# Kernel optimization log

Hardware: AMD Instinct MI355X
Metric: run time of the kernel (lower is better)

The kernel has to match this reference:

```python
import jax, jax.numpy as jnp
import numpy as np

B, T, N = 8, 1024, 1024
R, NR = 8, 128          # regions, neurons per region (N = R*NR)
D = 512                 # d_model


def setup_inputs() -> dict:
    key = jax.random.key(0)
    ks = jax.random.split(key, 6)
    spikes = jax.random.normal(ks[0], (B, T, N), dtype=jnp.float32)
    # region assignment: random permutation of neuron ids split into R groups
    perm = jax.random.permutation(ks[1], N)
    region_indices = perm.reshape(R, NR).astype(jnp.int32)
    # per-region Linear(NR -> D) stored already transposed for gathered layout
    W_enc = jax.random.normal(ks[2], (R, NR, D), dtype=jnp.float32) / np.sqrt(NR)
    b_enc = jax.random.normal(ks[3], (R, D), dtype=jnp.float32) * 0.02
    # per-region Linear(D -> NR)
    W_dec = jax.random.normal(ks[4], (R, D, NR), dtype=jnp.float32) / np.sqrt(D)
    b_dec = jax.random.normal(ks[5], (R, NR), dtype=jnp.float32) * 0.02
    return {"spikes": spikes, "W_enc": W_enc, "b_enc": b_enc,
            "W_dec": W_dec, "b_dec": b_dec, "region_indices": region_indices}


def reference(spikes, W_enc, b_enc, W_dec, b_dec, region_indices):
    # gather: per-region channel subsets  [B,T,R,NR]
    x_r = spikes[:, :, region_indices]
    # RegionEncoder: Linear(NR -> D) per region  [B,T,R,D]
    tokens = jnp.einsum('btrn,rnd->btrd', x_r, W_enc) + b_enc
    # RegionDecoder: Linear(D -> NR) per region  [B,T,R,NR]
    y = jnp.einsum('btrd,rdn->btrn', tokens, W_dec) + b_dec
    # scatter back into full neuron axis (index_copy_ on dim 2)
    flat_idx = region_indices.reshape(-1)          # [N], a permutation
    out = jnp.zeros_like(spikes).at[:, :, flat_idx].set(y.reshape(spikes.shape[0], spikes.shape[1], -1))
    return out
```

## Files before the change

### kernel.cpp

```cpp
#include <hip/hip_runtime.h>
#include <hip/hip_bf16.h>


typedef __attribute__((ext_vector_type(8))) short bf16x8;
typedef __attribute__((ext_vector_type(4))) float f32x4;
typedef __attribute__((ext_vector_type(4))) short s16x4;

#define NREG 8
#define NRD  128
#define DD   512
#define NN   1024
#define ROWS 16

static __device__ __forceinline__ unsigned short f2bf(float x) {
  union { float f; unsigned u; } v; v.f = x;
  unsigned r = v.u + 0x7fffu + ((v.u >> 16) & 1u);
  return (unsigned short)(r >> 16);
}
static __device__ __forceinline__ unsigned short f2bf_hw(float x) {
  union { __hip_bfloat16 h; unsigned short u; } c;
  c.h = __float2bfloat16(x);
  return c.u;
}
static __device__ __forceinline__ float bf2f(unsigned short b) {
  union { unsigned u; float f; } v; v.u = ((unsigned)b) << 16;
  return v.f;
}

__global__ __launch_bounds__(256) void prep1_kernel(
    const float* __restrict__ W_enc, const float* __restrict__ b_enc,
    const float* __restrict__ W_dec, const int* __restrict__ idx,
    int* __restrict__ pos_ws, float* __restrict__ part,
    float* __restrict__ part_c)
{
  __shared__ unsigned short As[128 * 128];
  __shared__ unsigned short Bs[128 * 128];
  int blk = blockIdx.x, t = threadIdx.x;

  if (blk < 32) {
    int r = blk >> 2, dc = blk & 3, d0 = dc * 128;
    const float* We = W_enc + (size_t)r * NRD * DD;
    const float* Wd = W_dec + (size_t)r * DD * NRD;
    const float* be = b_enc + (size_t)r * DD;

    int n4 = (t & 31) * 4, dlb = t >> 5;
    float c0 = 0.f, c1 = 0.f, c2 = 0.f, c3 = 0.f;
    #pragma unroll
    for (int p = 0; p < 16; ++p) {
      int dl = dlb + p * 8;
      float4 v = *(const float4*)&Wd[(size_t)(d0 + dl) * NRD + n4];
      float bev = be[d0 + dl];
      As[(n4 + 0) * 128 + (dl ^ (((n4 + 0) & 7) << 3))] = f2bf(v.x);
      As[(n4 + 1) * 128 + (dl ^ (((n4 + 1) & 7) << 3))] = f2bf(v.y);
      As[(n4 + 2) * 128 + (dl ^ (((n4 + 2) & 7) << 3))] = f2bf(v.z);
      As[(n4 + 3) * 128 + (dl ^ (((n4 + 3) & 7) << 3))] = f2bf(v.w);
      c0 += v.x * bev; c1 += v.y * bev; c2 += v.z * bev; c3 += v.w * bev;
    }
    {
      float4 cv; cv.x = c0; cv.y = c1; cv.z = c2; cv.w = c3;
      *(float4*)&part_c[((size_t)(r * 4 + dc) * 8 + dlb) * 128 + n4] = cv;
    }
    #pragma unroll
    for (int i = 0; i < 8; ++i) {
      int cid = t + i * 256;
      int k = cid >> 4, dq = (cid & 15) * 8;
      const float* src = &We[(size_t)k * DD + d0 + dq];
      float4 u = *(const float4*)src;
      float4 u2 = *(const float4*)(src + 4);
      bf16x8 pk;
      pk[0] = (short)f2bf(u.x);  pk[1] = (short)f2bf(u.y);
      pk[2] = (short)f2bf(u.z);  pk[3] = (short)f2bf(u.w);
      pk[4] = (short)f2bf(u2.x); pk[5] = (short)f2bf(u2.y);
      pk[6] = (short)f2bf(u2.z); pk[7] = (short)f2bf(u2.w);
      *(bf16x8*)&Bs[k * 128 + (dq ^ ((k & 7) << 3))] = pk;
    }
    __syncthreads();

    int lane = t & 63, w = t >> 6;
    int arow = lane & 15, ag = lane >> 4;
    f32x4 acc[8][2];
    #pragma unroll
    for (int i = 0; i < 8; ++i) {
      acc[i][0] = (f32x4){0.f, 0.f, 0.f, 0.f};
      acc[i][1] = (f32x4){0.f, 0.f, 0.f, 0.f};
    }
    #pragma unroll
    for (int nt = 0; nt < 8; ++nt) {
      int nl = nt * 16 + arow, asw = (nl & 7) << 3;
      bf16x8 a[4];
      #pragma unroll
      for (int ks = 0; ks < 4; ++ks)
        a[ks] = *(const bf16x8*)&As[nl * 128 + ((ks * 32 + ag * 8) ^ asw)];
      #pragma unroll
      for (int kt = 0; kt < 2; ++kt) {
        int kk = w * 32 + kt * 16 + arow, bsw = (kk & 7) << 3;
        #pragma unroll
        for (int ks = 0; ks < 4; ++ks) {
          bf16x8 b = *(const bf16x8*)&Bs[kk * 128 + ((ks * 32 + ag * 8) ^ bsw)];
          acc[nt][kt] = __builtin_amdgcn_mfma_f32_16x16x32_bf16(a[ks], b, acc[nt][kt], 0, 0, 0);
        }
      }
    }
    float* dst = part + (size_t)(r * 4 + dc) * 16384;
    #pragma unroll
    for (int nt = 0; nt < 8; ++nt)
      #pragma unroll
      for (int kt = 0; kt < 2; ++kt)
        #pragma unroll
        for (int v = 0; v < 4; ++v)
          dst[(nt * 16 + ag * 4 + v) * 128 + (w * 32 + kt * 16 + arow)] = acc[nt][kt][v];
  } else {
    #pragma unroll
    for (int i = 0; i < 4; ++i) {
      int q = t * 4 + i;
      pos_ws[idx[q]] = q;
    }
  }
}

__global__ __launch_bounds__(256) void prep2_kernel(
    const float* __restrict__ part, const float* __restrict__ part_c,
    const float* __restrict__ b_dec, unsigned short* __restrict__ MTp,
    float* __restrict__ c_ws)
{
  int blk = blockIdx.x, t = threadIdx.x;
  if (blk < 128) {
    int e0 = (blk * 256 + t) * 4;
    int r = e0 >> 14, off = e0 & 16383;
    int n = off >> 7, k0 = off & 127;
    const float* p = part + (size_t)r * 4 * 16384 + off;
    float4 s0 = *(const float4*)&p[0];
    float4 s1 = *(const float4*)&p[16384];
    float4 s2 = *(const float4*)&p[32768];
    float4 s3 = *(const float4*)&p[49152];
    s16x4 o;
    o.x = (short)f2bf(s0.x + s1.x + s2.x + s3.x);
    o.y = (short)f2bf(s0.y + s1.y + s2.y + s3.y);
    o.z = (short)f2bf(s0.z + s1.z + s2.z + s3.z);
    o.w = (short)f2bf(s0.w + s1.w + s2.w + s3.w);
    int w = n >> 4, arow = n & 15, kt = k0 >> 5, ag = (k0 >> 3) & 3, sub = k0 & 7;
    int chunk = (r * 32 + w * 4 + kt) * 64 + (arow * 4 + ag);
    *(s16x4*)&MTp[chunk * 8 + sub] = o;
  } else if (blk < 132) {
    int e = (blk - 128) * 256 + t;
    int n = e & 127;
    int r = e >> 7;
    float s = b_dec[e];
    #pragma unroll
    for (int dc = 0; dc < 4; ++dc)
      #pragma unroll
      for (int g = 0; g < 8; ++g)
        s += part_c[((size_t)(r * 4 + dc) * 8 + g) * 128 + n];
    c_ws[e] = s;
  }
}

__global__ __launch_bounds__(512, 4) void codec_kernel(
    const float* __restrict__ spikes, const int* __restrict__ pos_ws,
    const float* __restrict__ c_ws, const unsigned short* __restrict__ MTp,
    float* __restrict__ out)
{
  __shared__ unsigned short Xs[ROWS * NN];
  int t = threadIdx.x;
  int w = t >> 6, lane = t & 63;
  int arow = lane & 15, ag = lane >> 4;
  int asw = (arow & 7) << 3;
  int lanechunk = arow * 4 + ag;
  size_t row0 = (size_t)blockIdx.x * ROWS;
  const bf16x8* Bb = (const bf16x8*)MTp;

  int4 p4c[4];
  #pragma unroll
  for (int ch = 0; ch < 4; ++ch)
    p4c[ch] = *(const int4*)&pos_ws[ch * 256 + lane * 4];
  float cvr[8];
  #pragma unroll
  for (int j = 0; j < 8; ++j)
    cvr[j] = c_ws[w * 128 + j * 16 + arow];

  float4 sv[4][2];
  #pragma unroll
  for (int ch = 0; ch < 4; ++ch)
    #pragma unroll
    for (int rl = 0; rl < 2; ++rl)
      sv[ch][rl] = *(const float4*)&spikes[(row0 + w * 2 + rl) * NN + ch * 256 + lane * 4];

  bf16x8 bb[2][4];
  #pragma unroll
  for (int kt = 0; kt < 4; ++kt)
    bb[0][kt] = Bb[(w * 32 + 0 * 4 + kt) * 64 + lanechunk];
  #pragma unroll
  for (int kt = 0; kt < 4; ++kt)
    bb[1][kt] = Bb[(w * 32 + 1 * 4 + kt) * 64 + lanechunk];

  #pragma unroll
  for (int ch = 0; ch < 4; ++ch) {
    int4 p4 = p4c[ch];
    #pragma unroll
    for (int rl = 0; rl < 2; ++rl) {
      int row = w * 2 + rl;
      int base = row * NN, sw = (row & 7) << 3;
      float4 v = sv[ch][rl];
      Xs[base + (p4.x ^ sw)] = f2bf_hw(v.x);
      Xs[base + (p4.y ^ sw)] = f2bf_hw(v.y);
      Xs[base + (p4.z ^ sw)] = f2bf_hw(v.z);
      Xs[base + (p4.w ^ sw)] = f2bf_hw(v.w);
    }
  }
  __syncthreads();

  bf16x8 a[4];
  #pragma unroll
  for (int kt = 0; kt < 4; ++kt)
    a[kt] = *(const bf16x8*)&Xs[arow * NN + ((w * 128 + kt * 32 + ag * 8) ^ asw)];
  #pragma unroll
  for (int j = 0; j < 8; ++j) {
    f32x4 acc = {0.f, 0.f, 0.f, 0.f};
    #pragma unroll
    for (int kt = 0; kt < 4; ++kt)
      acc = __builtin_amdgcn_mfma_f32_16x16x32_bf16(a[kt], bb[j & 1][kt], acc, 0, 0, 0);
    if (j + 2 < 8) {
      #pragma unroll
      for (int kt = 0; kt < 4; ++kt)
        bb[j & 1][kt] = Bb[(w * 32 + (j + 2) * 4 + kt) * 64 + lanechunk];
    }
    int coln = w * 128 + j * 16 + arow;
    #pragma unroll
    for (int v = 0; v < 4; ++v) {
      int i = ag * 4 + v, isw = (i & 7) << 3;
      Xs[i * NN + (coln ^ isw)] = f2bf_hw(acc[v] + cvr[j]);
    }
  }
  __syncthreads();

  #pragma unroll
  for (int ch = 0; ch < 4; ++ch) {
    int j = ch * 256 + lane * 4;
    int4 p4 = p4c[ch];
    #pragma unroll
    for (int rl = 0; rl < 2; ++rl) {
      int row = w * 2 + rl;
      int base = row * NN, sw = (row & 7) << 3;
      float4 v;
      v.x = bf2f(Xs[base + (p4.x ^ sw)]);
      v.y = bf2f(Xs[base + (p4.y ^ sw)]);
      v.z = bf2f(Xs[base + (p4.z ^ sw)]);
      v.w = bf2f(Xs[base + (p4.w ^ sw)]);
      *(float4*)&out[(row0 + row) * NN + j] = v;
    }
  }
}

extern "C" void kernel_launch(void* const* d_in, const int* in_sizes, int n_in,
                              void* d_out, int out_size, void* d_ws, size_t ws_size,
                              hipStream_t stream) {
  const float* spikes = (const float*)d_in[0];
  const float* W_enc  = (const float*)d_in[1];
  const float* b_enc  = (const float*)d_in[2];
  const float* W_dec  = (const float*)d_in[3];
  const float* b_dec  = (const float*)d_in[4];
  const int*   idx    = (const int*)d_in[5];
  float* out = (float*)d_out;

  char* ws = (char*)d_ws;
  int*            pos_ws  = (int*)ws;
  float*          c_ws    = (float*)(ws + 4096);
  unsigned short* MTp_ws  = (unsigned short*)(ws + 8192);
  float*          part    = (float*)(ws + 270336);
  float*          part_c  = (float*)(ws + 2367488);

  prep1_kernel<<<33, 256, 0, stream>>>(W_enc, b_enc, W_dec, idx,
                                       pos_ws, part, part_c);
  prep2_kernel<<<132, 256, 0, stream>>>(part, part_c, b_dec, MTp_ws, c_ws);
  codec_kernel<<<8192 / ROWS, 512, 0, stream>>>(spikes, pos_ws, c_ws, MTp_ws, out);
}
```

Before: 31.91 us.

## Stage raw fp32 spikes in LDS via direct loads and gather at MFMA operand read

The codec kernel now copies each spike row straight into LDS as fp32 with global_load_lds. It then does the neuron-permutation gather while building the bf16 MFMA A operands, using region_indices directly instead of an inverse-permutation scatter. Decoder outputs are kept as fp32 in LDS at their scattered positions and streamed out with vector copies, which removes the per-element bf16 scatter and the bf16 round-trip on output. The cost is a doubled LDS footprint per block (64KB), which may cut the number of resident blocks per CU.

Result: slower. 32.78 us (+2.7%).

```diff
diff --git a/kernel.cpp b/kernel.cpp
--- a/kernel.cpp
+++ b/kernel.cpp
@@ -21,10 +21,6 @@
   union { __hip_bfloat16 h; unsigned short u; } c;
   c.h = __float2bfloat16(x);
   return c.u;
-}
-static __device__ __forceinline__ float bf2f(unsigned short b) {
-  union { unsigned u; float f; } v; v.u = ((unsigned)b) << 16;
-  return v.f;
 }
 
 __global__ __launch_bounds__(256) void prep1_kernel(
@@ -127,7 +123,6 @@
   if (blk < 128) {
     int e0 = (blk * 256 + t) * 4;
     int r = e0 >> 14, off = e0 & 16383;
-    int n = off >> 7, k0 = off & 127;
     const float* p = part + (size_t)r * 4 * 16384 + off;
     float4 s0 = *(const float4*)&p[0];
     float4 s1 = *(const float4*)&p[16384];
@@ -138,6 +133,7 @@
     o.y = (short)f2bf(s0.y + s1.y + s2.y + s3.y);
     o.z = (short)f2bf(s0.z + s1.z + s2.z + s3.z);
     o.w = (short)f2bf(s0.w + s1.w + s2.w + s3.w);
+    int n = off >> 7, k0 = off & 127;
     int w = n >> 4, arow = n & 15, kt = k0 >> 5, ag = (k0 >> 3) & 3, sub = k0 & 7;
     int chunk = (r * 32 + w * 4 + kt) * 64 + (arow * 4 + ag);
     *(s16x4*)&MTp[chunk * 8 + sub] = o;
@@ -156,35 +152,49 @@
 }
 
 __global__ __launch_bounds__(512, 4) void codec_kernel(
-    const float* __restrict__ spikes, const int* __restrict__ pos_ws,
+    const float* __restrict__ spikes, const int* __restrict__ idx,
     const float* __restrict__ c_ws, const unsigned short* __restrict__ MTp,
     float* __restrict__ out)
 {
-  __shared__ unsigned short Xs[ROWS * NN];
+  __shared__ float Xs[ROWS * NN];
   int t = threadIdx.x;
   int w = t >> 6, lane = t & 63;
   int arow = lane & 15, ag = lane >> 4;
-  int asw = (arow & 7) << 3;
+  int aswz = (arow & 7) << 2;
   int lanechunk = arow * 4 + ag;
   size_t row0 = (size_t)blockIdx.x * ROWS;
   const bf16x8* Bb = (const bf16x8*)MTp;
-
-  int4 p4c[4];
-  #pragma unroll
-  for (int ch = 0; ch < 4; ++ch)
-    p4c[ch] = *(const int4*)&pos_ws[ch * 256 + lane * 4];
+  const int* idxr = idx + w * 128;
+
+  #pragma unroll
+  for (int rl = 0; rl < 2; ++rl) {
+    int row = w * 2 + rl;
+    int sw = (row & 7) << 2;
+    const float* srow = &spikes[(row0 + row) * NN];
+    float* drow = &Xs[row * NN];
+    #pragma unroll
+    for (int ch = 0; ch < 4; ++ch) {
+      int u = ch * 256 + lane * 4;
+      __builtin_amdgcn_global_load_lds(
+          (const __attribute__((address_space(1))) void*)&srow[u ^ sw],
+          (__attribute__((address_space(3))) void*)&drow[ch * 256],
+          16, 0, 0);
+    }
+  }
+
+  int4 iv[4][2];
+  #pragma unroll
+  for (int kt = 0; kt < 4; ++kt) {
+    iv[kt][0] = *(const int4*)&idxr[kt * 32 + ag * 8];
+    iv[kt][1] = *(const int4*)&idxr[kt * 32 + ag * 8 + 4];
+  }
+  int colv[8];
   float cvr[8];
   #pragma unroll
-  for (int j = 0; j < 8; ++j)
-    cvr[j] = c_ws[w * 128 + j * 16 + arow];
-
-  float4 sv[4][2];
-  #pragma unroll
-  for (int ch = 0; ch < 4; ++ch)
-    #pragma unroll
-    for (int rl = 0; rl < 2; ++rl)
-      sv[ch][rl] = *(const float4*)&spikes[(row0 + w * 2 + rl) * NN + ch * 256 + lane * 4];
-
+  for (int j = 0; j < 8; ++j) {
+    colv[j] = idxr[j * 16 + arow];
+    cvr[j]  = c_ws[w * 128 + j * 16 + arow];
+  }
   bf16x8 bb[2][4];
   #pragma unroll
   for (int kt = 0; kt < 4; ++kt)
@@ -193,26 +203,25 @@
   for (int kt = 0; kt < 4; ++kt)
     bb[1][kt] = Bb[(w * 32 + 1 * 4 + kt) * 64 + lanechunk];
 
-  #pragma unroll
-  for (int ch = 0; ch < 4; ++ch) {
-    int4 p4 = p4c[ch];
-    #pragma unroll
-    for (int rl = 0; rl < 2; ++rl) {
-      int row = w * 2 + rl;
-      int base = row * NN, sw = (row & 7) << 3;
-      float4 v = sv[ch][rl];
-      Xs[base + (p4.x ^ sw)] = f2bf_hw(v.x);
-      Xs[base + (p4.y ^ sw)] = f2bf_hw(v.y);
-      Xs[base + (p4.z ^ sw)] = f2bf_hw(v.z);
-      Xs[base + (p4.w ^ sw)] = f2bf_hw(v.w);
-    }
-  }
   __syncthreads();
 
+  const float* arow_p = &Xs[arow * NN];
   bf16x8 a[4];
   #pragma unroll
-  for (int kt = 0; kt < 4; ++kt)
-    a[kt] = *(const bf16x8*)&Xs[arow * NN + ((w * 128 + kt * 32 + ag * 8) ^ asw)];
+  for (int kt = 0; kt < 4; ++kt) {
+    int4 i0 = iv[kt][0], i1 = iv[kt][1];
+    bf16x8 pk;
+    pk[0] = (short)f2bf_hw(arow_p[i0.x ^ aswz]);
+    pk[1] = (short)f2bf_hw(arow_p[i0.y ^ aswz]);
+    pk[2] = (short)f2bf_hw(arow_p[i0.z ^ aswz]);
+    pk[3] = (short)f2bf_hw(arow_p[i0.w ^ aswz]);
+    pk[4] = (short)f2bf_hw(arow_p[i1.x ^ aswz]);
+    pk[5] = (short)f2bf_hw(arow_p[i1.y ^ aswz]);
+    pk[6] = (short)f2bf_hw(arow_p[i1.z ^ aswz]);
+    pk[7] = (short)f2bf_hw(arow_p[i1.w ^ aswz]);
+    a[kt] = pk;
+  }
+
   #pragma unroll
   for (int j = 0; j < 8; ++j) {
     f32x4 acc = {0.f, 0.f, 0.f, 0.f};
@@ -224,29 +233,25 @@
       for (int kt = 0; kt < 4; ++kt)
         bb[j & 1][kt] = Bb[(w * 32 + (j + 2) * 4 + kt) * 64 + lanechunk];
     }
-    int coln = w * 128 + j * 16 + arow;
     #pragma unroll
     for (int v = 0; v < 4; ++v) {
-      int i = ag * 4 + v, isw = (i & 7) << 3;
-      Xs[i * NN + (coln ^ isw)] = f2bf_hw(acc[v] + cvr[j]);
+      int i = ag * 4 + v, isw = (i & 7) << 2;
+      Xs[i * NN + (colv[j] ^ isw)] = acc[v] + cvr[j];
     }
   }
   __syncthreads();
 
   #pragma unroll
-  for (int ch = 0; ch < 4; ++ch) {
-    int j = ch * 256 + lane * 4;
-    int4 p4 = p4c[ch];
-    #pragma unroll
-    for (int rl = 0; rl < 2; ++rl) {
-      int row = w * 2 + rl;
-      int base = row * NN, sw = (row & 7) << 3;
-      float4 v;
-      v.x = bf2f(Xs[base + (p4.x ^ sw)]);
-      v.y = bf2f(Xs[base + (p4.y ^ sw)]);
-      v.z = bf2f(Xs[base + (p4.z ^ sw)]);
-      v.w = bf2f(Xs[base + (p4.w ^ sw)]);
-      *(float4*)&out[(row0 + row) * NN + j] = v;
+  for (int rl = 0; rl < 2; ++rl) {
+    int row = w * 2 + rl;
+    int sw = (row & 7) << 2;
+    const float* srow = &Xs[row * NN];
+    float* orow = &out[(row0 + row) * NN];
+    #pragma unroll
+    for (int ch = 0; ch < 4; ++ch) {
+      int u = ch * 256 + lane * 4;
+      f32x4 v = *(const f32x4*)&srow[u ^ sw];
+      *(f32x4*)&orow[u] = v;
     }
   }
 }
@@ -272,5 +277,5 @@
   prep1_kernel<<<33, 256, 0, stream>>>(W_enc, b_enc, W_dec, idx,
                                        pos_ws, part, part_c);
   prep2_kernel<<<132, 256, 0, stream>>>(part, part_c, b_dec, MTp_ws, c_ws);
-  codec_kernel<<<8192 / ROWS, 512, 0, stream>>>(spikes, pos_ws, c_ws, MTp_ws, out);
-}
+  codec_kernel<<<8192 / ROWS, 512, 0, stream>>>(spikes, idx, c_ws, MTp_ws, out);
+}
```

## Fuse the two prep kernels by looping over the d-chunks inside each block

Applied to the files above, without the earlier changes.

The prep stage no longer splits the D=512 reduction across four blocks per region. Each block now owns a 32-column slice of n and loops over all four d-chunks, accumulating in registers. This removes the fp32 partial-product workspace and the second reduction kernel launch, and writes the packed bf16 matrix and the bias vector directly. The cost is that each block now reloads all of W_enc for its region, four times the previous per-block load work, and runs a serial d-loop with extra syncs.

After: 55.47 us. +73.8%, slower.

```diff
diff --git a/kernel.cpp b/kernel.cpp
--- a/kernel.cpp
+++ b/kernel.cpp
@@ -27,131 +27,105 @@
   return v.f;
 }
 
-__global__ __launch_bounds__(256) void prep1_kernel(
+__global__ __launch_bounds__(256) void prep_kernel(
     const float* __restrict__ W_enc, const float* __restrict__ b_enc,
-    const float* __restrict__ W_dec, const int* __restrict__ idx,
-    int* __restrict__ pos_ws, float* __restrict__ part,
-    float* __restrict__ part_c)
+    const float* __restrict__ W_dec, const float* __restrict__ b_dec,
+    const int* __restrict__ idx, int* __restrict__ pos_ws,
+    unsigned short* __restrict__ MTp, float* __restrict__ c_ws)
 {
-  __shared__ unsigned short As[128 * 128];
+  __shared__ unsigned short As[32 * 128];
   __shared__ unsigned short Bs[128 * 128];
+  __shared__ float cred[256];
   int blk = blockIdx.x, t = threadIdx.x;
 
   if (blk < 32) {
-    int r = blk >> 2, dc = blk & 3, d0 = dc * 128;
+    int r = blk >> 2, nq = blk & 3, n0 = nq * 32;
     const float* We = W_enc + (size_t)r * NRD * DD;
     const float* Wd = W_dec + (size_t)r * DD * NRD;
     const float* be = b_enc + (size_t)r * DD;
-
-    int n4 = (t & 31) * 4, dlb = t >> 5;
-    float c0 = 0.f, c1 = 0.f, c2 = 0.f, c3 = 0.f;
-    #pragma unroll
-    for (int p = 0; p < 16; ++p) {
-      int dl = dlb + p * 8;
-      float4 v = *(const float4*)&Wd[(size_t)(d0 + dl) * NRD + n4];
-      float bev = be[d0 + dl];
-      As[(n4 + 0) * 128 + (dl ^ (((n4 + 0) & 7) << 3))] = f2bf(v.x);
-      As[(n4 + 1) * 128 + (dl ^ (((n4 + 1) & 7) << 3))] = f2bf(v.y);
-      As[(n4 + 2) * 128 + (dl ^ (((n4 + 2) & 7) << 3))] = f2bf(v.z);
-      As[(n4 + 3) * 128 + (dl ^ (((n4 + 3) & 7) << 3))] = f2bf(v.w);
-      c0 += v.x * bev; c1 += v.y * bev; c2 += v.z * bev; c3 += v.w * bev;
-    }
-    {
-      float4 cv; cv.x = c0; cv.y = c1; cv.z = c2; cv.w = c3;
-      *(float4*)&part_c[((size_t)(r * 4 + dc) * 8 + dlb) * 128 + n4] = cv;
-    }
-    #pragma unroll
-    for (int i = 0; i < 8; ++i) {
-      int cid = t + i * 256;
-      int k = cid >> 4, dq = (cid & 15) * 8;
-      const float* src = &We[(size_t)k * DD + d0 + dq];
-      float4 u = *(const float4*)src;
-      float4 u2 = *(const float4*)(src + 4);
-      bf16x8 pk;
-      pk[0] = (short)f2bf(u.x);  pk[1] = (short)f2bf(u.y);
-      pk[2] = (short)f2bf(u.z);  pk[3] = (short)f2bf(u.w);
-      pk[4] = (short)f2bf(u2.x); pk[5] = (short)f2bf(u2.y);
-      pk[6] = (short)f2bf(u2.z); pk[7] = (short)f2bf(u2.w);
-      *(bf16x8*)&Bs[k * 128 + (dq ^ ((k & 7) << 3))] = pk;
-    }
-    __syncthreads();
-
     int lane = t & 63, w = t >> 6;
     int arow = lane & 15, ag = lane >> 4;
-    f32x4 acc[8][2];
-    #pragma unroll
-    for (int i = 0; i < 8; ++i) {
-      acc[i][0] = (f32x4){0.f, 0.f, 0.f, 0.f};
-      acc[i][1] = (f32x4){0.f, 0.f, 0.f, 0.f};
-    }
-    #pragma unroll
-    for (int nt = 0; nt < 8; ++nt) {
-      int nl = nt * 16 + arow, asw = (nl & 7) << 3;
-      bf16x8 a[4];
-      #pragma unroll
-      for (int ks = 0; ks < 4; ++ks)
-        a[ks] = *(const bf16x8*)&As[nl * 128 + ((ks * 32 + ag * 8) ^ asw)];
-      #pragma unroll
-      for (int kt = 0; kt < 2; ++kt) {
-        int kk = w * 32 + kt * 16 + arow, bsw = (kk & 7) << 3;
+    int cn = t & 31, dlb = t >> 5;
+
+    float cp = 0.f;
+    f32x4 acc[2][2];
+    acc[0][0] = (f32x4){0.f, 0.f, 0.f, 0.f};
+    acc[0][1] = (f32x4){0.f, 0.f, 0.f, 0.f};
+    acc[1][0] = (f32x4){0.f, 0.f, 0.f, 0.f};
+    acc[1][1] = (f32x4){0.f, 0.f, 0.f, 0.f};
+
+    for (int dc = 0; dc < 4; ++dc) {
+      int d0 = dc * 128;
+      #pragma unroll
+      for (int p = 0; p < 16; ++p) {
+        int dl = dlb + p * 8;
+        float v = Wd[(size_t)(d0 + dl) * NRD + n0 + cn];
+        As[cn * 128 + (dl ^ ((cn & 7) << 3))] = f2bf(v);
+        cp += v * be[d0 + dl];
+      }
+      #pragma unroll
+      for (int i = 0; i < 8; ++i) {
+        int cid = t + i * 256;
+        int k = cid >> 4, dq = (cid & 15) * 8;
+        const float* src = &We[(size_t)k * DD + d0 + dq];
+        float4 u = *(const float4*)src;
+        float4 u2 = *(const float4*)(src + 4);
+        bf16x8 pk;
+        pk[0] = (short)f2bf(u.x);  pk[1] = (short)f2bf(u.y);
+        pk[2] = (short)f2bf(u.z);  pk[3] = (short)f2bf(u.w);
+        pk[4] = (short)f2bf(u2.x); pk[5] = (short)f2bf(u2.y);
+        pk[6] = (short)f2bf(u2.z); pk[7] = (short)f2bf(u2.w);
+        *(bf16x8*)&Bs[k * 128 + (dq ^ ((k & 7) << 3))] = pk;
+      }
+      __syncthreads();
+
+      #pragma unroll
+      for (int nt = 0; nt < 2; ++nt) {
+        int nl = nt * 16 + arow, asw = (nl & 7) << 3;
+        bf16x8 a[4];
         #pragma unroll
-        for (int ks = 0; ks < 4; ++ks) {
-          bf16x8 b = *(const bf16x8*)&Bs[kk * 128 + ((ks * 32 + ag * 8) ^ bsw)];
-          acc[nt][kt] = __builtin_amdgcn_mfma_f32_16x16x32_bf16(a[ks], b, acc[nt][kt], 0, 0, 0);
+        for (int ks = 0; ks < 4; ++ks)
+          a[ks] = *(const bf16x8*)&As[nl * 128 + ((ks * 32 + ag * 8) ^ asw)];
+        #pragma unroll
+        for (int kt = 0; kt < 2; ++kt) {
+          int kk = w * 32 + kt * 16 + arow, bsw = (kk & 7) << 3;
+          #pragma unroll
+          for (int ks = 0; ks < 4; ++ks) {
+            bf16x8 b = *(const bf16x8*)&Bs[kk * 128 + ((ks * 32 + ag * 8) ^ bsw)];
+            acc[nt][kt] = __builtin_amdgcn_mfma_f32_16x16x32_bf16(a[ks], b, acc[nt][kt], 0, 0, 0);
+          }
         }
       }
-    }
-    float* dst = part + (size_t)(r * 4 + dc) * 16384;
-    #pragma unroll
-    for (int nt = 0; nt < 8; ++nt)
+      __syncthreads();
+    }
+
+    #pragma unroll
+    for (int nt = 0; nt < 2; ++nt)
       #pragma unroll
       for (int kt = 0; kt < 2; ++kt)
         #pragma unroll
-        for (int v = 0; v < 4; ++v)
-          dst[(nt * 16 + ag * 4 + v) * 128 + (w * 32 + kt * 16 + arow)] = acc[nt][kt][v];
+        for (int v = 0; v < 4; ++v) {
+          int n = n0 + nt * 16 + ag * 4 + v;
+          int k = w * 32 + kt * 16 + arow;
+          int chunk = (r * 32 + (n >> 4) * 4 + (k >> 5)) * 64 + ((n & 15) * 4 + ((k >> 3) & 3));
+          MTp[(size_t)chunk * 8 + (k & 7)] = f2bf(acc[nt][kt][v]);
+        }
+
+    cred[t] = cp;
+    __syncthreads();
+    if (t < 32) {
+      float s = b_dec[r * NRD + n0 + t];
+      #pragma unroll
+      for (int g = 0; g < 8; ++g)
+        s += cred[g * 32 + t];
+      c_ws[r * NRD + n0 + t] = s;
+    }
   } else {
     #pragma unroll
     for (int i = 0; i < 4; ++i) {
       int q = t * 4 + i;
       pos_ws[idx[q]] = q;
     }
-  }
-}
-
-__global__ __launch_bounds__(256) void prep2_kernel(
-    const float* __restrict__ part, const float* __restrict__ part_c,
-    const float* __restrict__ b_dec, unsigned short* __restrict__ MTp,
-    float* __restrict__ c_ws)
-{
-  int blk = blockIdx.x, t = threadIdx.x;
-  if (blk < 128) {
-    int e0 = (blk * 256 + t) * 4;
-    int r = e0 >> 14, off = e0 & 16383;
-    int n = off >> 7, k0 = off & 127;
-    const float* p = part + (size_t)r * 4 * 16384 + off;
-    float4 s0 = *(const float4*)&p[0];
-    float4 s1 = *(const float4*)&p[16384];
-    float4 s2 = *(const float4*)&p[32768];
-    float4 s3 = *(const float4*)&p[49152];
-    s16x4 o;
-    o.x = (short)f2bf(s0.x + s1.x + s2.x + s3.x);
-    o.y = (short)f2bf(s0.y + s1.y + s2.y + s3.y);
-    o.z = (short)f2bf(s0.z + s1.z + s2.z + s3.z);
-    o.w = (short)f2bf(s0.w + s1.w + s2.w + s3.w);
-    int w = n >> 4, arow = n & 15, kt = k0 >> 5, ag = (k0 >> 3) & 3, sub = k0 & 7;
-    int chunk = (r * 32 + w * 4 + kt) * 64 + (arow * 4 + ag);
-    *(s16x4*)&MTp[chunk * 8 + sub] = o;
-  } else if (blk < 132) {
-    int e = (blk - 128) * 256 + t;
-    int n = e & 127;
-    int r = e >> 7;
-    float s = b_dec[e];
-    #pragma unroll
-    for (int dc = 0; dc < 4; ++dc)
-      #pragma unroll
-      for (int g = 0; g < 8; ++g)
-        s += part_c[((size_t)(r * 4 + dc) * 8 + g) * 128 + n];
-    c_ws[e] = s;
   }
 }
 
@@ -263,14 +237,11 @@
   float* out = (float*)d_out;
 
   char* ws = (char*)d_ws;
-  int*            pos_ws  = (int*)ws;
-  float*          c_ws    = (float*)(ws + 4096);
-  unsigned short* MTp_ws  = (unsigned short*)(ws + 8192);
-  float*          part    = (float*)(ws + 270336);
-  float*          part_c  = (float*)(ws + 2367488);
-
-  prep1_kernel<<<33, 256, 0, stream>>>(W_enc, b_enc, W_dec, idx,
-                                       pos_ws, part, part_c);
-  prep2_kernel<<<132, 256, 0, stream>>>(part, part_c, b_dec, MTp_ws, c_ws);
+  int*            pos_ws = (int*)ws;
+  float*          c_ws   = (float*)(ws + 4096);
+  unsigned short* MTp_ws = (unsigned short*)(ws + 8192);
+
+  prep_kernel<<<33, 256, 0, stream>>>(W_enc, b_enc, W_dec, b_dec, idx,
+                                      pos_ws, MTp_ws, c_ws);
   codec_kernel<<<8192 / ROWS, 512, 0, stream>>>(spikes, pos_ws, c_ws, MTp_ws, out);
 }
```
